# Performance work log

Hardware: AMD Instinct MI355X
Metric: run time of the kernel (lower is better)

## Reference

```python
import jax, jax.numpy as jnp
import numpy as np

EPS = 1e-7
NUM_ROUTING = 3


def squash(s, axis=-1):
    # v = ||s||^2/(1+||s||^2) * s/||s||, numerically safe
    sq = jnp.sum(jnp.square(s), axis=axis, keepdims=True)
    scale = sq / (1.0 + sq) / jnp.sqrt(sq + EPS)
    return scale * s


def setup_inputs() -> dict:
    key = jax.random.key(0)
    k1, k2 = jax.random.split(key)
    B, IN_CAPS, IN_DIM = 256, 1152, 8
    NUM_CAPS, DIM_VEC = 10, 16
    inputs = jax.random.normal(k1, (B, IN_CAPS, IN_DIM), dtype=jnp.float32)
    # glorot_uniform over [in_caps, num_caps, dim_vec, in_dim]
    limit = np.sqrt(6.0 / (IN_DIM + DIM_VEC))
    W = jax.random.uniform(k2, (IN_CAPS, NUM_CAPS, DIM_VEC, IN_DIM), dtype=jnp.float32,
                           minval=-limit, maxval=limit)
    bias = jnp.zeros((IN_CAPS, NUM_CAPS), dtype=jnp.float32)
    return {"inputs": inputs, "W": W, "bias": bias}


def reference(inputs, W, bias):
    # u_hat[b,i,c,d] = W[i,c,d,e] @ inputs[b,i,e]
    u_hat = jnp.einsum('icde,bie->bicd', W, inputs)  # [B, in_caps, num_caps, dim_vec]
    b = bias[None]  # [1, in_caps, num_caps], broadcasts to [B, ...]
    for _ in range(NUM_ROUTING - 1):
        c = jax.nn.softmax(b, axis=2)                       # over num_capsule
        s = jnp.einsum('bic,bicd->bcd', c * jnp.ones_like(u_hat[..., 0]), u_hat)
        v = squash(s, axis=-1)                              # [B, num_caps, dim_vec]
        agreement = jnp.einsum('bicd,bcd->bic', u_hat, v)
        b = agreement + b + bias[None]
    c_last = jax.nn.softmax(b, axis=2)
    s = jnp.einsum('bic,bicd->bcd', c_last * jnp.ones_like(u_hat[..., 0]), u_hat)
    outputs = squash(s, axis=-1)                            # [B, num_caps, dim_vec]
    return outputs
```

## Files before the change

### kernel.cpp

```cpp
#include <hip/hip_runtime.h>
#include <math.h>

#define BATCH 256
#define IC    1152
#define EDIM  8
#define NC    10
#define DV    16

#define ITILE  8
#define NCHUNK 4
#define ITOT   (ITILE * NCHUNK)
#define NB     4
#define NTHREADS 256
#define NWAVES 4
#define NSLAB  (IC / ITOT)
#define BCHUNKS (BATCH / NB)
#define SCD (NC * DV)
#define SPART_STRIDE (BATCH * SCD)

template<int CTRL>
__device__ __forceinline__ float dpp_add(float x) {
    int r = __builtin_amdgcn_update_dpp(0, __float_as_int(x), CTRL, 0xF, 0xF, true);
    return x + __int_as_float(r);
}
__device__ __forceinline__ float row_reduce16(float x) {
    x = dpp_add<0xB1>(x);
    x = dpp_add<0x4E>(x);
    x = dpp_add<0x141>(x);
    x = dpp_add<0x140>(x);
    return x;
}

template<int MODE>
__global__ __launch_bounds__(NTHREADS, 2)
void caps_main(const float* __restrict__ x,
               const float* __restrict__ W,
               const float* __restrict__ bias,
               const float* __restrict__ v_in,
               float* __restrict__ b2,
               float* __restrict__ s_part)
{
    __shared__ float sx[NB][ITOT * EDIM];
    __shared__ float swv[NWAVES][NB][SCD];

    const int tid = threadIdx.x;
    const int d   = tid & 15;
    const int ch  = (tid >> 4) & 1;
    const int il  = tid >> 5;
    const int wid = tid >> 6;
    const int icb = blockIdx.x;
    const int bcb = blockIdx.y;
    const int i0  = icb * ITOT;
    const int b0  = bcb * NB;

    {
        const float4* xg = (const float4*)x;
        float4* xs = (float4*)&sx[0][0];
        int bb = tid >> 6;
        int w  = tid & 63;
        xs[tid] = xg[(size_t)(b0 + bb) * (IC * EDIM / 4) + i0 * (EDIM / 4) + w];
    }

    float sacc[NB][5];
    #pragma unroll
    for (int bb = 0; bb < NB; ++bb)
        #pragma unroll
        for (int k = 0; k < 5; ++k) sacc[bb][k] = 0.f;

    __syncthreads();

    const float4* Wg = (const float4*)W;

    #pragma unroll 1
    for (int ic = 0; ic < NCHUNK; ++ic) {
        const int i = i0 + ic * ITILE + il;

        float4 w4[5][2];
        float  bv[5];
        #pragma unroll
        for (int k = 0; k < 5; ++k) {
            int c = ch * 5 + k;
            size_t base = ((size_t)(i * NC + c) * DV + d) * 2;
            w4[k][0] = Wg[base];
            w4[k][1] = Wg[base + 1];
            bv[k]    = bias[i * NC + c];
        }

        float cw[5];
        if (MODE == 1) {
            float mx = fmaxf(fmaxf(fmaxf(bv[0], bv[1]), fmaxf(bv[2], bv[3])), bv[4]);
            mx = fmaxf(mx, __shfl_xor(mx, 16));
            float ssum = 0.f, ex[5];
            #pragma unroll
            for (int k = 0; k < 5; ++k) { ex[k] = __expf(bv[k] - mx); ssum += ex[k]; }
            ssum += __shfl_xor(ssum, 16);
            float inv = 1.0f / ssum;
            #pragma unroll
            for (int k = 0; k < 5; ++k) cw[k] = ex[k] * inv;
        }

        #pragma unroll
        for (int bb = 0; bb < NB; ++bb) {
            const int b = b0 + bb;
            const float4 x0 = ((const float4*)&sx[bb][(ic * ITILE + il) * EDIM])[0];
            const float4 x1 = ((const float4*)&sx[bb][(ic * ITILE + il) * EDIM])[1];

            float u[5];
            #pragma unroll
            for (int k = 0; k < 5; ++k) {
                float acc = w4[k][0].x * x0.x;
                acc = fmaf(w4[k][0].y, x0.y, acc);
                acc = fmaf(w4[k][0].z, x0.z, acc);
                acc = fmaf(w4[k][0].w, x0.w, acc);
                acc = fmaf(w4[k][1].x, x1.x, acc);
                acc = fmaf(w4[k][1].y, x1.y, acc);
                acc = fmaf(w4[k][1].z, x1.z, acc);
                acc = fmaf(w4[k][1].w, x1.w, acc);
                u[k] = acc;
            }

            if (MODE != 1) {
                const float* vb = v_in + (size_t)b * SCD + ch * 80 + d;
                float t[5];
                #pragma unroll
                for (int k = 0; k < 5; ++k) t[k] = u[k] * vb[k * 16];
                #pragma unroll
                for (int k = 0; k < 5; ++k) t[k] = row_reduce16(t[k]);

                float br[5];
                float* bp = b2 + (((size_t)b * IC + i) * 2 + ch) * 8;
                if (MODE == 2) {
                    #pragma unroll
                    for (int k = 0; k < 5; ++k) br[k] = t[k] + 2.0f * bv[k];
                    if (d == 0) {
                        #pragma unroll
                        for (int k = 0; k < 5; ++k) bp[k] = br[k];
                    }
                } else {
                    #pragma unroll
                    for (int k = 0; k < 5; ++k) br[k] = t[k] + bp[k] + bv[k];
                }
                float mx = fmaxf(fmaxf(fmaxf(br[0], br[1]), fmaxf(br[2], br[3])), br[4]);
                mx = fmaxf(mx, __shfl_xor(mx, 16));
                float ssum = 0.f, ex[5];
                #pragma unroll
                for (int k = 0; k < 5; ++k) { ex[k] = __expf(br[k] - mx); ssum += ex[k]; }
                ssum += __shfl_xor(ssum, 16);
                float inv = 1.0f / ssum;
                #pragma unroll
                for (int k = 0; k < 5; ++k) cw[k] = ex[k] * inv;
            }

            #pragma unroll
            for (int k = 0; k < 5; ++k)
                sacc[bb][k] = fmaf(cw[k], u[k], sacc[bb][k]);
        }
    }

    #pragma unroll
    for (int bb = 0; bb < NB; ++bb) {
        #pragma unroll
        for (int k = 0; k < 5; ++k) {
            float s = sacc[bb][k] + __shfl_xor(sacc[bb][k], 32);
            if ((tid & 32) == 0)
                swv[wid][bb][ch * 80 + k * 16 + d] = s;
        }
    }
    __syncthreads();
    for (int j = tid; j < NB * SCD; j += NTHREADS) {
        int bb = j / SCD;
        int cd = j - bb * SCD;
        float s = (swv[0][bb][cd] + swv[1][bb][cd])
                + (swv[2][bb][cd] + swv[3][bb][cd]);
        s_part[((size_t)icb * BATCH + b0 + bb) * SCD + cd] = s;
    }
}

__global__ __launch_bounds__(256)
void caps_squash(const float* __restrict__ s_part, float* __restrict__ out)
{
    const int tid = threadIdx.x;
    const int bc  = blockIdx.x * 16 + (tid >> 4);
    const size_t off = (size_t)bc * DV + (tid & 15);

    float a[4] = {0.f, 0.f, 0.f, 0.f};
    #pragma unroll
    for (int ic = 0; ic < NSLAB; ic += 4) {
        #pragma unroll
        for (int j = 0; j < 4; ++j)
            a[j] += s_part[(size_t)(ic + j) * SPART_STRIDE + off];
    }
    float s = (a[0] + a[1]) + (a[2] + a[3]);

    float sq = row_reduce16(s * s);

    float scale = sq / ((1.0f + sq) * sqrtf(sq + 1e-7f));
    out[off] = scale * s;
}

extern "C" void kernel_launch(void* const* d_in, const int* in_sizes, int n_in,
                              void* d_out, int out_size, void* d_ws, size_t ws_size,
                              hipStream_t stream)
{
    const float* x    = (const float*)d_in[0];
    const float* W    = (const float*)d_in[1];
    const float* bias = (const float*)d_in[2];
    float* out = (float*)d_out;

    float* ws     = (float*)d_ws;
    float* s_part = ws;
    float* v      = s_part + (size_t)NSLAB * SPART_STRIDE;
    float* b2     = v + SPART_STRIDE;

    dim3 grid(NSLAB, BCHUNKS);

    caps_main<1><<<grid, NTHREADS, 0, stream>>>(x, W, bias, v, b2, s_part);
    caps_squash<<<160, 256, 0, stream>>>(s_part, v);
    caps_main<2><<<grid, NTHREADS, 0, stream>>>(x, W, bias, v, b2, s_part);
    caps_squash<<<160, 256, 0, stream>>>(s_part, v);
    caps_main<3><<<grid, NTHREADS, 0, stream>>>(x, W, bias, v, b2, s_part);
    caps_squash<<<160, 256, 0, stream>>>(s_part, out);
}
```

Measured before the change: 183.2 us.

## Halve slab size, remap blocks per XCD, stage v and b2 in LDS, drop softmax max

```diff
diff --git a/kernel.cpp b/kernel.cpp
--- a/kernel.cpp
+++ b/kernel.cpp
@@ -8,7 +8,7 @@
 #define DV    16
 
 #define ITILE  8
-#define NCHUNK 4
+#define NCHUNK 2
 #define ITOT   (ITILE * NCHUNK)
 #define NB     4
 #define NTHREADS 256
@@ -41,6 +41,8 @@
                float* __restrict__ s_part)
 {
     __shared__ float sx[NB][ITOT * EDIM];
+    __shared__ float sv[NB][SCD];
+    __shared__ float sb2[NB][ITOT * 16];
     __shared__ float swv[NWAVES][NB][SCD];
 
     const int tid = threadIdx.x;
@@ -48,17 +50,32 @@
     const int ch  = (tid >> 4) & 1;
     const int il  = tid >> 5;
     const int wid = tid >> 6;
-    const int icb = blockIdx.x;
-    const int bcb = blockIdx.y;
+
+    const int bid = blockIdx.x;
+    const int xcd = bid & 7;
+    const int grp = bid >> 3;
+    const int icb = xcd * 9 + (grp % 9);
+    const int bcb = grp / 9;
     const int i0  = icb * ITOT;
     const int b0  = bcb * NB;
 
-    {
+    if (tid < NB * ITOT * EDIM / 4) {
         const float4* xg = (const float4*)x;
-        float4* xs = (float4*)&sx[0][0];
+        int bb = tid >> 5;
+        int w  = tid & 31;
+        ((float4*)&sx[0][0])[tid] =
+            xg[(size_t)(b0 + bb) * (IC * EDIM / 4) + i0 * (EDIM / 4) + w];
+    }
+    if (MODE != 1) {
+        if (tid < NB * SCD / 4)
+            ((float4*)&sv[0][0])[tid] =
+                ((const float4*)v_in)[(size_t)b0 * (SCD / 4) + tid];
+    }
+    if (MODE == 3) {
+        const float4* bg = (const float4*)b2;
         int bb = tid >> 6;
         int w  = tid & 63;
-        xs[tid] = xg[(size_t)(b0 + bb) * (IC * EDIM / 4) + i0 * (EDIM / 4) + w];
+        ((float4*)&sb2[0][0])[tid] = bg[((size_t)(b0 + bb) * IC + i0) * 4 + w];
     }
 
     float sacc[NB][5];
@@ -72,8 +89,8 @@
     const float4* Wg = (const float4*)W;
 
     #pragma unroll 1
-    for (int ic = 0; ic < NCHUNK; ++ic) {
-        const int i = i0 + ic * ITILE + il;
+    for (int icl = 0; icl < NCHUNK; ++icl) {
+        const int i = i0 + icl * ITILE + il;
 
         float4 w4[5][2];
         float  bv[5];
@@ -88,11 +105,9 @@
 
         float cw[5];
         if (MODE == 1) {
-            float mx = fmaxf(fmaxf(fmaxf(bv[0], bv[1]), fmaxf(bv[2], bv[3])), bv[4]);
-            mx = fmaxf(mx, __shfl_xor(mx, 16));
             float ssum = 0.f, ex[5];
             #pragma unroll
-            for (int k = 0; k < 5; ++k) { ex[k] = __expf(bv[k] - mx); ssum += ex[k]; }
+            for (int k = 0; k < 5; ++k) { ex[k] = __expf(bv[k]); ssum += ex[k]; }
             ssum += __shfl_xor(ssum, 16);
             float inv = 1.0f / ssum;
             #pragma unroll
@@ -101,9 +116,8 @@
 
         #pragma unroll
         for (int bb = 0; bb < NB; ++bb) {
-            const int b = b0 + bb;
-            const float4 x0 = ((const float4*)&sx[bb][(ic * ITILE + il) * EDIM])[0];
-            const float4 x1 = ((const float4*)&sx[bb][(ic * ITILE + il) * EDIM])[1];
+            const float4 x0 = ((const float4*)&sx[bb][(icl * ITILE + il) * EDIM])[0];
+            const float4 x1 = ((const float4*)&sx[bb][(icl * ITILE + il) * EDIM])[1];
 
             float u[5];
             #pragma unroll
@@ -120,31 +134,30 @@
             }
 
             if (MODE != 1) {
-                const float* vb = v_in + (size_t)b * SCD + ch * 80 + d;
                 float t[5];
                 #pragma unroll
-                for (int k = 0; k < 5; ++k) t[k] = u[k] * vb[k * 16];
+                for (int k = 0; k < 5; ++k)
+                    t[k] = u[k] * sv[bb][ch * 80 + k * 16 + d];
                 #pragma unroll
                 for (int k = 0; k < 5; ++k) t[k] = row_reduce16(t[k]);
 
                 float br[5];
-                float* bp = b2 + (((size_t)b * IC + i) * 2 + ch) * 8;
                 if (MODE == 2) {
                     #pragma unroll
                     for (int k = 0; k < 5; ++k) br[k] = t[k] + 2.0f * bv[k];
                     if (d == 0) {
+                        float* bp = b2 + (((size_t)(b0 + bb) * IC + i) * 2 + ch) * 8;
                         #pragma unroll
                         for (int k = 0; k < 5; ++k) bp[k] = br[k];
                     }
                 } else {
+                    const float* bp = &sb2[bb][(icl * ITILE + il) * 16 + ch * 8];
                     #pragma unroll
                     for (int k = 0; k < 5; ++k) br[k] = t[k] + bp[k] + bv[k];
                 }
-                float mx = fmaxf(fmaxf(fmaxf(br[0], br[1]), fmaxf(br[2], br[3])), br[4]);
-                mx = fmaxf(mx, __shfl_xor(mx, 16));
                 float ssum = 0.f, ex[5];
                 #pragma unroll
-                for (int k = 0; k < 5; ++k) { ex[k] = __expf(br[k] - mx); ssum += ex[k]; }
+                for (int k = 0; k < 5; ++k) { ex[k] = __expf(br[k]); ssum += ex[k]; }
                 ssum += __shfl_xor(ssum, 16);
                 float inv = 1.0f / ssum;
                 #pragma unroll
@@ -183,14 +196,14 @@
     const int bc  = blockIdx.x * 16 + (tid >> 4);
     const size_t off = (size_t)bc * DV + (tid & 15);
 
-    float a[4] = {0.f, 0.f, 0.f, 0.f};
+    float a[8] = {0.f, 0.f, 0.f, 0.f, 0.f, 0.f, 0.f, 0.f};
     #pragma unroll
-    for (int ic = 0; ic < NSLAB; ic += 4) {
-        #pragma unroll
-        for (int j = 0; j < 4; ++j)
+    for (int ic = 0; ic < NSLAB; ic += 8) {
+        #pragma unroll
+        for (int j = 0; j < 8; ++j)
             a[j] += s_part[(size_t)(ic + j) * SPART_STRIDE + off];
     }
-    float s = (a[0] + a[1]) + (a[2] + a[3]);
+    float s = ((a[0] + a[1]) + (a[2] + a[3])) + ((a[4] + a[5]) + (a[6] + a[7]));
 
     float sq = row_reduce16(s * s);
 
@@ -212,7 +225,7 @@
     float* v      = s_part + (size_t)NSLAB * SPART_STRIDE;
     float* b2     = v + SPART_STRIDE;
 
-    dim3 grid(NSLAB, BCHUNKS);
+    const int grid = NSLAB * BCHUNKS;
 
     caps_main<1><<<grid, NTHREADS, 0, stream>>>(x, W, bias, v, b2, s_part);
     caps_squash<<<160, 256, 0, stream>>>(s_part, v);
```

Result: slower. 198.3 us (+8.2%).
